# Performance work log

Measured on AMD Instinct MI355X. Metric: run time of the kernel, lower is better.

The kernel has to match this reference:

```python
import jax, jax.numpy as jnp
import numpy as np

B, C, H, W = 8, 512, 64, 64
R = 16
CQK = C // R  # 32


def setup_inputs() -> dict:
    key = jax.random.key(0)
    kx, kq, kk, kv = jax.random.split(key, 4)
    x = jax.random.normal(kx, (B, C, H, W), dtype=jnp.float32)
    # Conv1d with kernel_size=1, bias=False == matmul over channel dim
    Wq = jax.random.normal(kq, (CQK, C), dtype=jnp.float32) * (1.0 / np.sqrt(C))
    Wk = jax.random.normal(kk, (CQK, C), dtype=jnp.float32) * (1.0 / np.sqrt(C))
    Wv = jax.random.normal(kv, (C, C), dtype=jnp.float32) * (1.0 / np.sqrt(C))
    return {"x": x, "Wq": Wq, "Wk": Wk, "Wv": Wv}


def reference(x, Wq, Wk, Wv):
    b, c, h, w = x.shape
    xf = x.reshape(b, c, h * w)                 # [b, c, n]
    q = jnp.einsum('dc,bcn->bdn', Wq, xf)       # [b, c/r, n]
    k = jnp.einsum('dc,bcn->bdn', Wk, xf)       # [b, c/r, n]
    attn = jax.nn.softmax(jnp.einsum('bdm,bdn->bmn', q, k), axis=-1)  # [b, n, n]
    v = jnp.einsum('dc,bcn->bdn', Wv, xf)       # [b, c, n]
    out = jnp.einsum('bcm,bmn->bcn', v, attn)   # [b, c, n]
    return out.reshape(b, c, h, w)
```

## Files before the change

### kernel.cpp

```cpp
#include <hip/hip_runtime.h>
#include <hip/hip_bf16.h>


typedef __attribute__((ext_vector_type(8))) short s16x8;
typedef __attribute__((ext_vector_type(4))) float f32x4;

#define MFMA16(a, b, c) __builtin_amdgcn_mfma_f32_16x16x32_bf16((a), (b), (c), 0, 0, 0)

__device__ __forceinline__ ushort f2bf(float f) {
  union { float f; unsigned u; } v; v.f = f;
  return (ushort)((v.u + 0x8000u) >> 16);
}
__device__ __forceinline__ unsigned pack_bf16(float lo, float hi) {
  union { float f; unsigned u; } a, b; a.f = lo; b.f = hi;
  return __builtin_amdgcn_perm(b.u + 0x8000u, a.u + 0x8000u, 0x07060302u);
}

__global__ void k_cvt_w(const float* __restrict__ Wq, const float* __restrict__ Wk,
                        const float* __restrict__ Wv, ushort* __restrict__ Wqb,
                        ushort* __restrict__ Wkb, ushort* __restrict__ Wvb) {
  int i = blockIdx.x * 256 + threadIdx.x;
  if (i < 262144) Wvb[i] = f2bf(Wv[i]);
  else if (i < 278528) Wqb[i - 262144] = f2bf(Wq[i - 262144] * 1.4426950408889634f);
  else if (i < 294912) Wkb[i - 278528] = f2bf(Wk[i - 278528]);
}

__global__ __launch_bounds__(256) void k_xpose(const float* __restrict__ x,
                                               ushort* __restrict__ xT) {
  const int b = blockIdx.z, c0 = blockIdx.y * 64, n0 = blockIdx.x * 256;
  __shared__ uint U[2][64][65];
  const int t = threadIdx.x;
  const int wv = t >> 6, ln = t & 63;
  const float* xp = x + ((size_t)b * 512 + c0 + wv * 16) * 4096 + n0 + ln * 4;
#pragma unroll
  for (int i = 0; i < 16; ++i) {
    float4 f = *(const float4*)(xp + (size_t)i * 4096);
    U[0][wv * 16 + i][ln] = pack_bf16(f.x, f.y);
    U[1][wv * 16 + i][ln] = pack_bf16(f.z, f.w);
  }
  __syncthreads();
  const int c_seg = (t & 7) * 8;
#pragma unroll
  for (int pass = 0; pass < 8; ++pass) {
    const int nl = pass * 32 + (t >> 3);
    const int p = nl >> 1;
    const int h = p & 1, idx = p >> 1;
    const uint sel = (nl & 1) ? 0x07060302u : 0x05040100u;
    uint o[4];
#pragma unroll
    for (int j = 0; j < 4; ++j) {
      uint ua = U[h][c_seg + 2 * j][idx];
      uint ub = U[h][c_seg + 2 * j + 1][idx];
      o[j] = __builtin_amdgcn_perm(ub, ua, sel);
    }
    *(uint4*)(xT + ((size_t)b * 4096 + n0 + nl) * 512 + c0 + c_seg) = *(uint4*)o;
  }
}

__global__ __launch_bounds__(256, 2) void k_proj(const ushort* __restrict__ xT,
                                                 const ushort* __restrict__ Wqb,
                                                 const ushort* __restrict__ Wkb,
                                                 const ushort* __restrict__ Wvb,
                                                 ushort* __restrict__ qb,
                                                 ushort* __restrict__ kb,
                                                 ushort* __restrict__ vb) {
  const int b = blockIdx.y, n0 = blockIdx.x * 64;
  const int lane = threadIdx.x & 63, w = threadIdx.x >> 6;
  const int quad = lane >> 4, l15 = lane & 15;
  const ushort* xT_b = xT + (size_t)b * 4096 * 512;

  const ushort* Wqk = (w < 2) ? (Wqb + (size_t)(w * 16 + l15) * 512)
                              : (Wkb + (size_t)((w - 2) * 16 + l15) * 512);

  f32x4 accv[8][4], accqk[4];
#pragma unroll
  for (int i = 0; i < 8; ++i)
#pragma unroll
    for (int nt = 0; nt < 4; ++nt) accv[i][nt] = {0.f, 0.f, 0.f, 0.f};
#pragma unroll
  for (int nt = 0; nt < 4; ++nt) accqk[nt] = {0.f, 0.f, 0.f, 0.f};

  for (int k0 = 0; k0 < 512; k0 += 32) {
    s16x8 bx[4];
#pragma unroll
    for (int nt = 0; nt < 4; ++nt)
      bx[nt] = *(const s16x8*)(xT_b + (size_t)(n0 + nt * 16 + l15) * 512 + k0 + quad * 8);
#pragma unroll
    for (int i = 0; i < 8; ++i) {
      s16x8 av = *(const s16x8*)(Wvb + (size_t)((8 * w + i) * 16 + l15) * 512 + k0 + quad * 8);
#pragma unroll
      for (int nt = 0; nt < 4; ++nt) accv[i][nt] = MFMA16(av, bx[nt], accv[i][nt]);
    }
    s16x8 aqk = *(const s16x8*)(Wqk + k0 + quad * 8);
#pragma unroll
    for (int nt = 0; nt < 4; ++nt) accqk[nt] = MFMA16(aqk, bx[nt], accqk[nt]);
  }

  ushort* vb_b = vb + (size_t)b * 512 * 4096;
#pragma unroll
  for (int i = 0; i < 8; ++i)
#pragma unroll
    for (int nt = 0; nt < 4; ++nt)
#pragma unroll
      for (int r = 0; r < 4; ++r)
        vb_b[(size_t)((8 * w + i) * 16 + quad * 4 + r) * 4096 + n0 + nt * 16 + l15] =
            f2bf(accv[i][nt][r]);

  ushort* qk_out = (w < 2) ? (qb + (size_t)b * 4096 * 32) : (kb + (size_t)b * 4096 * 32);
#pragma unroll
  for (int nt = 0; nt < 4; ++nt) {
    ushort4 u;
    u.x = f2bf(accqk[nt][0]); u.y = f2bf(accqk[nt][1]);
    u.z = f2bf(accqk[nt][2]); u.w = f2bf(accqk[nt][3]);
    *(ushort4*)(qk_out + (size_t)(n0 + nt * 16 + l15) * 32 + (w & 1) * 16 + quad * 4) = u;
  }
}

__global__ __launch_bounds__(256) void k_pass1(const ushort* __restrict__ qb,
                                               const ushort* __restrict__ kb,
                                               float* __restrict__ Lneg) {
  const int b = blockIdx.y, mt = blockIdx.x;
  const int lane = threadIdx.x & 63, w = threadIdx.x >> 6;
  const int quad = lane >> 4, l15 = lane & 15;
  const int m = mt * 64 + w * 16;
  const ushort* qb_b = qb + (size_t)b * 4096 * 32;
  const ushort* kb_b = kb + (size_t)b * 4096 * 32;
  const s16x8 aqf = *(const s16x8*)(qb_b + (size_t)(m + l15) * 32 + quad * 8);
  float ps[4] = {0.f, 0.f, 0.f, 0.f};
  const f32x4 zf = {0.f, 0.f, 0.f, 0.f};
  for (int n0 = 0; n0 < 4096; n0 += 64) {
#pragma unroll
    for (int nt = 0; nt < 4; ++nt) {
      s16x8 bk = *(const s16x8*)(kb_b + (size_t)(n0 + nt * 16 + l15) * 32 + quad * 8);
      f32x4 s = MFMA16(aqf, bk, zf);
#pragma unroll
      for (int r = 0; r < 4; ++r) ps[r] += exp2f(s[r]);
    }
  }
  for (int off = 1; off < 16; off <<= 1)
#pragma unroll
    for (int r = 0; r < 4; ++r) ps[r] += __shfl_xor(ps[r], off, 64);
  if (l15 == 0)
#pragma unroll
    for (int r = 0; r < 4; ++r)
      Lneg[(size_t)b * 4096 + m + quad * 4 + r] = -log2f(ps[r]);
}

__global__ __launch_bounds__(256, 2) void k_pass2(const ushort* __restrict__ qb,
                                                  const ushort* __restrict__ kb,
                                                  const ushort* __restrict__ vb,
                                                  const float* __restrict__ Lneg,
                                                  float* __restrict__ out) {
  const int blk = blockIdx.x;
  const int b = blk & 7, blkb = blk >> 3;
  const int ntb = blkb & 31, cb = blkb >> 5;
  const int nbase = ntb * 128;
  const int lane = threadIdx.x & 63, w = threadIdx.x >> 6;
  const int quad = lane >> 4, l15 = lane & 15;
  const int wm = w & 1, wn = w >> 1;
  const int cbase = cb * 256 + w * 64;
  const int swz = l15 & 7;

  __shared__ __align__(16) ushort PT[2][128 * 64];

  const ushort* qb_b = qb + (size_t)b * 4096 * 32;
  const ushort* kb_b = kb + (size_t)b * 4096 * 32;
  const ushort* vb_b = vb + (size_t)b * 512 * 4096;
  const float* L_b = Lneg + (size_t)b * 4096;

  s16x8 kf[4];
#pragma unroll
  for (int i = 0; i < 4; ++i)
    kf[i] = *(const s16x8*)(kb_b + (size_t)(nbase + (4 * wn + i) * 16 + l15) * 32 + quad * 8);

  f32x4 acc[4][8];
#pragma unroll
  for (int ci = 0; ci < 4; ++ci)
#pragma unroll
    for (int nt = 0; nt < 8; ++nt) acc[ci][nt] = {0.f, 0.f, 0.f, 0.f};

  s16x8 aqp[2];
  float4 l4p[2];
  s16x8 va[4][2];

  auto loadQ = [&](int chunk) {
    const int m0 = chunk * 64;
#pragma unroll
    for (int j = 0; j < 2; ++j) {
      const int M = 2 * wm + j;
      aqp[j] = *(const s16x8*)(qb_b + (size_t)(m0 + M * 16 + l15) * 32 + quad * 8);
      l4p[j] = *(const float4*)(L_b + m0 + M * 16 + quad * 4);
    }
  };
  auto loadV = [&](int chunk) {
    const int m0 = chunk * 64;
#pragma unroll
    for (int ci = 0; ci < 4; ++ci) {
      const ushort* vrow = vb_b + (size_t)(cbase + ci * 16 + l15) * 4096 + m0;
      va[ci][0] = *(const s16x8*)(vrow + quad * 8);
      va[ci][1] = *(const s16x8*)(vrow + 32 + quad * 8);
    }
  };
  auto produce_tile = [&](int buf, int j, int i) {
    char* Pw = (char*)&PT[buf][0];
    const int M = 2 * wm + j;
    const int T = 4 * wn + i;
    f32x4 cin; cin.x = l4p[j].x; cin.y = l4p[j].y; cin.z = l4p[j].z; cin.w = l4p[j].w;
    f32x4 s = MFMA16(aqp[j], kf[i], cin);
    uint2 u;
    u.x = pack_bf16(exp2f(s.x), exp2f(s.y));
    u.y = pack_bf16(exp2f(s.z), exp2f(s.w));
    const int row = T * 16 + l15;
    const int gran = (2 * M + (quad >> 1)) ^ swz;
    *(uint2*)(Pw + row * 128 + gran * 16 + (quad & 1) * 8) = u;
  };

  loadQ(0);
#pragma unroll
  for (int j = 0; j < 2; ++j)
#pragma unroll
    for (int i = 0; i < 4; ++i) produce_tile(0, j, i);
  loadQ(1);
  loadV(0);

  for (int chunk = 0; chunk < 64; ++chunk) {
    const int buf = chunk & 1;
    __syncthreads();
    const char* P = (const char*)&PT[buf][0];
    s16x8 p0[4], p1[4];
#pragma unroll
    for (int nt = 0; nt < 4; ++nt) {
      const int row = nt * 16 + l15;
      p0[nt] = *(const s16x8*)(P + row * 128 + (quad ^ swz) * 16);
      p1[nt] = *(const s16x8*)(P + row * 128 + ((4 + quad) ^ swz) * 16);
    }
#pragma unroll
    for (int nt = 0; nt < 4; ++nt) {
#pragma unroll
      for (int ci = 0; ci < 4; ++ci) {
        acc[ci][nt] = MFMA16(va[ci][0], p0[nt], acc[ci][nt]);
        acc[ci][nt] = MFMA16(va[ci][1], p1[nt], acc[ci][nt]);
      }
      produce_tile(buf ^ 1, 0, nt);
    }
    s16x8 r0[4], r1[4];
#pragma unroll
    for (int nt = 0; nt < 4; ++nt) {
      const int row = (nt + 4) * 16 + l15;
      r0[nt] = *(const s16x8*)(P + row * 128 + (quad ^ swz) * 16);
      r1[nt] = *(const s16x8*)(P + row * 128 + ((4 + quad) ^ swz) * 16);
    }
#pragma unroll
    for (int nt = 0; nt < 4; ++nt) {
#pragma unroll
      for (int ci = 0; ci < 4; ++ci) {
        acc[ci][nt + 4] = MFMA16(va[ci][0], r0[nt], acc[ci][nt + 4]);
        acc[ci][nt + 4] = MFMA16(va[ci][1], r1[nt], acc[ci][nt + 4]);
      }
      produce_tile(buf ^ 1, 1, nt);
    }
    if (chunk < 62) loadQ(chunk + 2);
    if (chunk < 63) loadV(chunk + 1);
  }

  float* out_b = out + (size_t)b * 512 * 4096;
#pragma unroll
  for (int ci = 0; ci < 4; ++ci)
#pragma unroll
    for (int nt = 0; nt < 8; ++nt) {
      const int n = nbase + nt * 16 + l15;
      const int c0 = cbase + ci * 16 + quad * 4;
#pragma unroll
      for (int r = 0; r < 4; ++r) out_b[(size_t)(c0 + r) * 4096 + n] = acc[ci][nt][r];
    }
}

extern "C" void kernel_launch(void* const* d_in, const int* in_sizes, int n_in,
                              void* d_out, int out_size, void* d_ws, size_t ws_size,
                              hipStream_t stream) {
  const float* x  = (const float*)d_in[0];
  const float* Wq = (const float*)d_in[1];
  const float* Wk = (const float*)d_in[2];
  const float* Wv = (const float*)d_in[3];
  float* out = (float*)d_out;

  char* ws = (char*)d_ws;
  ushort* vb  = (ushort*)(ws + 0);
  ushort* xT  = (ushort*)(ws + 33554432);
  ushort* qb  = (ushort*)(ws + 67108864);
  ushort* kb  = (ushort*)(ws + 69206016);
  ushort* Wvb = (ushort*)(ws + 71303168);
  ushort* Wqb = (ushort*)(ws + 71827456);
  ushort* Wkb = (ushort*)(ws + 71860224);
  float*  Lrs = (float*)(ws + 71892992);

  hipLaunchKernelGGL(k_cvt_w, dim3(1152), dim3(256), 0, stream, Wq, Wk, Wv, Wqb, Wkb, Wvb);
  hipLaunchKernelGGL(k_xpose, dim3(16, 8, 8), dim3(256), 0, stream, x, xT);
  hipLaunchKernelGGL(k_proj, dim3(64, 8), dim3(256), 0, stream, xT, Wqb, Wkb, Wvb, qb, kb, vb);
  hipLaunchKernelGGL(k_pass1, dim3(64, 8), dim3(256), 0, stream, qb, kb, Lrs);
  hipLaunchKernelGGL(k_pass2, dim3(512), dim3(256), 0, stream, qb, kb, vb, Lrs, out);
}
```

Baseline: 388.9 us.

## Cover all channels per pass2 block with 512 threads, halving P recompute

Pass2 blocks now use 512 threads (8 waves) and cover all 512 channels for a 128-column tile, so the exp(QK) tile P is produced once per column tile instead of once per 256-channel half. Each wave now produces 4 P subtiles instead of 8, which removes redundant QK MFMAs and exponentials across blocks. The grid shrinks to 256 blocks, which may reduce occupancy and load balance on the CUs. The libm exp2f calls are also replaced by the hardware exp2 builtin, trading edge-case precision for fewer instructions.

```diff
diff --git a/kernel.cpp b/kernel.cpp
--- a/kernel.cpp
+++ b/kernel.cpp
@@ -15,6 +15,7 @@
   union { float f; unsigned u; } a, b; a.f = lo; b.f = hi;
   return __builtin_amdgcn_perm(b.u + 0x8000u, a.u + 0x8000u, 0x07060302u);
 }
+__device__ __forceinline__ float fexp2(float x) { return __builtin_amdgcn_exp2f(x); }
 
 __global__ void k_cvt_w(const float* __restrict__ Wq, const float* __restrict__ Wk,
                         const float* __restrict__ Wv, ushort* __restrict__ Wqb,
@@ -134,7 +135,7 @@
       s16x8 bk = *(const s16x8*)(kb_b + (size_t)(n0 + nt * 16 + l15) * 32 + quad * 8);
       f32x4 s = MFMA16(aqf, bk, zf);
 #pragma unroll
-      for (int r = 0; r < 4; ++r) ps[r] += exp2f(s[r]);
+      for (int r = 0; r < 4; ++r) ps[r] += fexp2(s[r]);
     }
   }
   for (int off = 1; off < 16; off <<= 1)
@@ -146,20 +147,20 @@
       Lneg[(size_t)b * 4096 + m + quad * 4 + r] = -log2f(ps[r]);
 }
 
-__global__ __launch_bounds__(256, 2) void k_pass2(const ushort* __restrict__ qb,
+__global__ __launch_bounds__(512, 2) void k_pass2(const ushort* __restrict__ qb,
                                                   const ushort* __restrict__ kb,
                                                   const ushort* __restrict__ vb,
                                                   const float* __restrict__ Lneg,
                                                   float* __restrict__ out) {
   const int blk = blockIdx.x;
-  const int b = blk & 7, blkb = blk >> 3;
-  const int ntb = blkb & 31, cb = blkb >> 5;
+  const int b = blk & 7, ntb = blk >> 3;
   const int nbase = ntb * 128;
   const int lane = threadIdx.x & 63, w = threadIdx.x >> 6;
   const int quad = lane >> 4, l15 = lane & 15;
-  const int wm = w & 1, wn = w >> 1;
-  const int cbase = cb * 256 + w * 64;
+  const int cbase = w * 64;
   const int swz = l15 & 7;
+  const int Mw = w >> 1;
+  const int Tb = (w & 1) * 4;
 
   __shared__ __align__(16) ushort PT[2][128 * 64];
 
@@ -171,7 +172,7 @@
   s16x8 kf[4];
 #pragma unroll
   for (int i = 0; i < 4; ++i)
-    kf[i] = *(const s16x8*)(kb_b + (size_t)(nbase + (4 * wn + i) * 16 + l15) * 32 + quad * 8);
+    kf[i] = *(const s16x8*)(kb_b + (size_t)(nbase + (Tb + i) * 16 + l15) * 32 + quad * 8);
 
   f32x4 acc[4][8];
 #pragma unroll
@@ -179,18 +180,14 @@
 #pragma unroll
     for (int nt = 0; nt < 8; ++nt) acc[ci][nt] = {0.f, 0.f, 0.f, 0.f};
 
-  s16x8 aqp[2];
-  float4 l4p[2];
+  s16x8 aqp;
+  float4 l4p;
   s16x8 va[4][2];
 
   auto loadQ = [&](int chunk) {
     const int m0 = chunk * 64;
-#pragma unroll
-    for (int j = 0; j < 2; ++j) {
-      const int M = 2 * wm + j;
-      aqp[j] = *(const s16x8*)(qb_b + (size_t)(m0 + M * 16 + l15) * 32 + quad * 8);
-      l4p[j] = *(const float4*)(L_b + m0 + M * 16 + quad * 4);
-    }
+    aqp = *(const s16x8*)(qb_b + (size_t)(m0 + Mw * 16 + l15) * 32 + quad * 8);
+    l4p = *(const float4*)(L_b + m0 + Mw * 16 + quad * 4);
   };
   auto loadV = [&](int chunk) {
     const int m0 = chunk * 64;
@@ -201,25 +198,22 @@
       va[ci][1] = *(const s16x8*)(vrow + 32 + quad * 8);
     }
   };
-  auto produce_tile = [&](int buf, int j, int i) {
+  auto produce_tile = [&](int buf, int i) {
     char* Pw = (char*)&PT[buf][0];
-    const int M = 2 * wm + j;
-    const int T = 4 * wn + i;
-    f32x4 cin; cin.x = l4p[j].x; cin.y = l4p[j].y; cin.z = l4p[j].z; cin.w = l4p[j].w;
-    f32x4 s = MFMA16(aqp[j], kf[i], cin);
+    const int T = Tb + i;
+    f32x4 cin; cin.x = l4p.x; cin.y = l4p.y; cin.z = l4p.z; cin.w = l4p.w;
+    f32x4 s = MFMA16(aqp, kf[i], cin);
     uint2 u;
-    u.x = pack_bf16(exp2f(s.x), exp2f(s.y));
-    u.y = pack_bf16(exp2f(s.z), exp2f(s.w));
+    u.x = pack_bf16(fexp2(s.x), fexp2(s.y));
+    u.y = pack_bf16(fexp2(s.z), fexp2(s.w));
     const int row = T * 16 + l15;
-    const int gran = (2 * M + (quad >> 1)) ^ swz;
+    const int gran = (2 * Mw + (quad >> 1)) ^ swz;
     *(uint2*)(Pw + row * 128 + gran * 16 + (quad & 1) * 8) = u;
   };
 
   loadQ(0);
 #pragma unroll
-  for (int j = 0; j < 2; ++j)
-#pragma unroll
-    for (int i = 0; i < 4; ++i) produce_tile(0, j, i);
+  for (int i = 0; i < 4; ++i) produce_tile(0, i);
   loadQ(1);
   loadV(0);
 
@@ -241,7 +235,7 @@
         acc[ci][nt] = MFMA16(va[ci][0], p0[nt], acc[ci][nt]);
         acc[ci][nt] = MFMA16(va[ci][1], p1[nt], acc[ci][nt]);
       }
-      produce_tile(buf ^ 1, 0, nt);
+      if (nt < 2) produce_tile(buf ^ 1, nt);
     }
     s16x8 r0[4], r1[4];
 #pragma unroll
@@ -257,7 +251,7 @@
         acc[ci][nt + 4] = MFMA16(va[ci][0], r0[nt], acc[ci][nt + 4]);
         acc[ci][nt + 4] = MFMA16(va[ci][1], r1[nt], acc[ci][nt + 4]);
       }
-      produce_tile(buf ^ 1, 1, nt);
+      if (nt < 2) produce_tile(buf ^ 1, nt + 2);
     }
     if (chunk < 62) loadQ(chunk + 2);
     if (chunk < 63) loadV(chunk + 1);
@@ -298,5 +292,5 @@
   hipLaunchKernelGGL(k_xpose, dim3(16, 8, 8), dim3(256), 0, stream, x, xT);
   hipLaunchKernelGGL(k_proj, dim3(64, 8), dim3(256), 0, stream, xT, Wqb, Wkb, Wvb, qb, kb, vb);
   hipLaunchKernelGGL(k_pass1, dim3(64, 8), dim3(256), 0, stream, qb, kb, Lrs);
-  hipLaunchKernelGGL(k_pass2, dim3(512), dim3(256), 0, stream, qb, kb, vb, Lrs, out);
-}
+  hipLaunchKernelGGL(k_pass2, dim3(256), dim3(512), 0, stream, qb, kb, vb, Lrs, out);
+}
```

New measurement: 363.3 us. 1.07x faster.
